# Optimization experiments

Hardware: AMD Instinct MI355X
Metric: run time of the kernel (lower is better)

## Reference

```python
import jax, jax.numpy as jnp
import numpy as np

EPS = 1e-5
COMMITMENT_WEIGHT = 1.0


def setup_inputs() -> dict:
    key = jax.random.key(0)
    k1, k2 = jax.random.split(key)
    x = jax.random.normal(k1, (4, 4096, 128), dtype=jnp.float32)
    codebook = jax.random.normal(k2, (8192, 128), dtype=jnp.float32)
    return {"x": x, "codebook": codebook}


def _layernorm(x):
    # LayerNorm over last dim, elementwise_affine=False, eps=1e-5
    mu = jnp.mean(x, axis=-1, keepdims=True)
    var = jnp.mean(jnp.square(x - mu), axis=-1, keepdims=True)
    return (x - mu) * jax.lax.rsqrt(var + EPS)


def reference(x, codebook):
    b, n, d = x.shape
    xn = _layernorm(x)                      # [b, n, d]
    flat = xn.reshape(b * n, d)             # [bn, d]
    x2 = jnp.sum(flat * flat, axis=-1, keepdims=True)          # [bn, 1]
    e2 = jnp.sum(codebook * codebook, axis=-1)                  # [K]
    dots = jnp.einsum('nd,kd->nk', flat, codebook)              # [bn, K]
    distances = x2 - 2.0 * dots + e2[None, :]                   # [bn, K]
    embed_ind = jnp.argmin(distances, axis=-1)                  # [bn]
    quantize = codebook[embed_ind].reshape(b, n, d)             # gather
    embed_ind = embed_ind.reshape(b, n)
    loss = jnp.mean(jnp.square(quantize - xn)) * COMMITMENT_WEIGHT
    # straight-through
    quantize_st = xn + jax.lax.stop_gradient(quantize - xn)
    return (quantize_st, embed_ind, loss)
```

## Files before the change

kernel.cpp:

```cpp
#include <hip/hip_runtime.h>
#include <hip/hip_fp16.h>
#include <math.h>

typedef _Float16 half8  __attribute__((ext_vector_type(8)));
typedef _Float16 half2v __attribute__((ext_vector_type(2)));
typedef float   floatx4 __attribute__((ext_vector_type(4)));

#define ROWS   16384
#define DIM    128
#define KCODES 8192
#define NSPLIT 16
#define MTILE  512
#define NT     64
#define NCHUNK ((KCODES / NSPLIT) / NT)
#define LOSS_SCALE (1.0f / ((float)ROWS * (float)DIM))

__device__ __forceinline__ void async_copy16(const _Float16* src, _Float16* dst_lds) {
  __builtin_amdgcn_global_load_lds((const __attribute__((address_space(1))) void*)src,
                                   (__attribute__((address_space(3))) void*)dst_lds,
                                   16, 0, 0);
}

__global__ __launch_bounds__(256) void prep_codebook(
    const float* __restrict__ cb, _Float16* __restrict__ ehg,
    _Float16* __restrict__ elg, float* __restrict__ e2g)
{
  int tid = threadIdx.x;
  int L = tid & 63;
  int row = blockIdx.x * 4 + (tid >> 6);
  const float2* cr = (const float2*)(cb + (size_t)row * DIM);
  float2 v = cr[L];
  float s2 = v.x * v.x + v.y * v.y;
  #pragma unroll
  for (int m = 1; m < 64; m <<= 1) s2 += __shfl_xor(s2, m);
  if (L == 0) e2g[row] = -0.5f * s2;
  _Float16 h0 = (_Float16)v.x, h1 = (_Float16)v.y;
  half2v hi = {h0, h1};
  half2v lo = {(_Float16)(v.x - (float)h0), (_Float16)(v.y - (float)h1)};
  ((half2v*)(ehg + (size_t)row * DIM))[L] = hi;
  ((half2v*)(elg + (size_t)row * DIM))[L] = lo;
}

__global__ __launch_bounds__(512, 2) void argmin_kernel(
    const float* __restrict__ x, const _Float16* __restrict__ ehg,
    const _Float16* __restrict__ elg, const float* __restrict__ e2g,
    float* __restrict__ best_part, int* __restrict__ idx_part,
    float* __restrict__ x2g)
{
  __shared__ _Float16 ebuf[2][2][64][128];
  __shared__ float e2s[KCODES / NSPLIT];

  int tid = threadIdx.x;
  int w   = tid >> 6;
  int L   = tid & 63;
  int c   = L & 15;
  int q   = L >> 4;

  int bx = blockIdx.x;
  int mt = bx & 31;
  int ns = bx >> 5;

  int rowbase = mt * MTILE + w * 64;
  int code0 = ns * (KCODES / NSPLIT);

  e2s[tid] = e2g[code0 + tid];

  half8 ah[4][4], al[4][4];

  #pragma unroll
  for (int g = 0; g < 4; ++g) {
    const float* xr = x + (size_t)(rowbase + g * 16 + c) * DIM;
    float v[32];
    #pragma unroll
    for (int ks = 0; ks < 4; ++ks) {
      float4 p0 = *(const float4*)(xr + ks * 32 + q * 8);
      float4 p1 = *(const float4*)(xr + ks * 32 + q * 8 + 4);
      v[ks*8+0] = p0.x; v[ks*8+1] = p0.y; v[ks*8+2] = p0.z; v[ks*8+3] = p0.w;
      v[ks*8+4] = p1.x; v[ks*8+5] = p1.y; v[ks*8+6] = p1.z; v[ks*8+7] = p1.w;
    }
    float s = 0.f;
    #pragma unroll
    for (int i = 0; i < 32; ++i) s += v[i];
    s += __shfl_xor(s, 16); s += __shfl_xor(s, 32);
    float mu = s * (1.0f / 128.0f);
    float s2 = 0.f;
    #pragma unroll
    for (int i = 0; i < 32; ++i) { float d = v[i] - mu; s2 += d * d; }
    s2 += __shfl_xor(s2, 16); s2 += __shfl_xor(s2, 32);
    float rstd = 1.0f / sqrtf(s2 * (1.0f / 128.0f) + 1e-5f);
    float x2 = 0.f;
    #pragma unroll
    for (int ks = 0; ks < 4; ++ks)
      #pragma unroll
      for (int j = 0; j < 8; ++j) {
        float xv = (v[ks*8+j] - mu) * rstd;
        x2 += xv * xv;
        _Float16 h = (_Float16)xv;
        ah[g][ks][j] = h;
        al[g][ks][j] = (_Float16)(xv - (float)h);
      }
    x2 += __shfl_xor(x2, 16); x2 += __shfl_xor(x2, 32);
    if (ns == 0 && q == 0) x2g[rowbase + g * 16 + c] = x2;
  }

  float best[4][4]; int bidx[4][4];
  #pragma unroll
  for (int g = 0; g < 4; ++g)
    #pragma unroll
    for (int r = 0; r < 4; ++r) { best[g][r] = -3.4e38f; bidx[g][r] = 0; }

  _Float16* lbase = &ebuf[0][0][0][0];

  auto stage = [&](int ch, int p) {
    int cbase = code0 + ch * NT;
    _Float16* lb = lbase + (size_t)p * 2 * 64 * 128;
    #pragma unroll
    for (int it = 0; it < 4; ++it) {
      int cid = it * 512 + tid;
      int arr = cid >> 10;
      int lc  = cid & 1023;
      int n   = lc >> 4;
      int kcs = lc & 15;
      int kc  = kcs ^ (n & 7);
      const _Float16* g = (arr ? elg : ehg) + (size_t)(cbase + n) * DIM + kc * 8;
      async_copy16(g, lb + (size_t)cid * 8);
    }
  };

  stage(0, 0);
  __syncthreads();

  for (int ch = 0; ch < NCHUNK; ++ch) {
    int p = ch & 1;
    int cbase = code0 + ch * NT;
    if (ch + 1 < NCHUNK) stage(ch + 1, p ^ 1);

    float e2h[4];
    #pragma unroll
    for (int s = 0; s < 4; ++s) e2h[s] = e2s[ch * NT + s * 16 + c];

    #pragma unroll
    for (int s = 0; s < 4; ++s) {
      int n = s * 16 + c;
      half8 bh[4], bl[4];
      #pragma unroll
      for (int ks = 0; ks < 4; ++ks) {
        int slot = ((ks * 4 + q) ^ (c & 7)) * 8;
        bh[ks] = *(const half8*)&ebuf[p][0][n][slot];
        bl[ks] = *(const half8*)&ebuf[p][1][n][slot];
      }
      int nn = cbase + n;
      #pragma unroll
      for (int g = 0; g < 4; ++g) {
        floatx4 acc = {e2h[s], e2h[s], e2h[s], e2h[s]};
        #pragma unroll
        for (int ks = 0; ks < 4; ++ks) {
          acc = __builtin_amdgcn_mfma_f32_16x16x32_f16(ah[g][ks], bh[ks], acc, 0, 0, 0);
          acc = __builtin_amdgcn_mfma_f32_16x16x32_f16(ah[g][ks], bl[ks], acc, 0, 0, 0);
          acc = __builtin_amdgcn_mfma_f32_16x16x32_f16(al[g][ks], bh[ks], acc, 0, 0, 0);
        }
        #pragma unroll
        for (int r = 0; r < 4; ++r) {
          float t = acc[r];
          if (t > best[g][r]) { best[g][r] = t; bidx[g][r] = nn; }
        }
      }
    }
    __syncthreads();
  }

  #pragma unroll
  for (int m = 1; m < 16; m <<= 1)
    #pragma unroll
    for (int g = 0; g < 4; ++g)
      #pragma unroll
      for (int r = 0; r < 4; ++r) {
        float ob = __shfl_xor(best[g][r], m);
        int   oi = __shfl_xor(bidx[g][r], m);
        if (ob > best[g][r] || (ob == best[g][r] && oi < bidx[g][r])) {
          best[g][r] = ob; bidx[g][r] = oi;
        }
      }
  if (c == 0) {
    #pragma unroll
    for (int g = 0; g < 4; ++g)
      #pragma unroll
      for (int r = 0; r < 4; ++r) {
        int row = rowbase + g * 16 + q * 4 + r;
        best_part[(size_t)row * NSPLIT + ns] = best[g][r];
        idx_part [(size_t)row * NSPLIT + ns] = bidx[g][r];
      }
  }
}

__global__ __launch_bounds__(256) void gather_loss_kernel(
    const float* __restrict__ cb, const float* __restrict__ best_part,
    const int* __restrict__ idx_part, const float* __restrict__ x2g,
    float* __restrict__ out_q, float* __restrict__ out_ind,
    float* __restrict__ out_loss)
{
  __shared__ int   sidx[32];
  __shared__ float sloss[32];
  int tid = threadIdx.x;
  int rb = blockIdx.x * 32;
  int r = tid >> 3, k = tid & 7;
  int row = rb + r;

  float b  = best_part[(size_t)row * NSPLIT + k];
  int   bi = idx_part [(size_t)row * NSPLIT + k];
  float b2 = best_part[(size_t)row * NSPLIT + 8 + k];
  int   bj = idx_part [(size_t)row * NSPLIT + 8 + k];
  if (b2 > b || (b2 == b && bj < bi)) { b = b2; bi = bj; }
  #pragma unroll
  for (int m = 1; m < 8; m <<= 1) {
    float ob = __shfl_xor(b, m);
    int   oi = __shfl_xor(bi, m);
    if (ob > b || (ob == b && oi < bi)) { b = ob; bi = oi; }
  }
  if (k == 0) {
    sidx[r] = bi;
    out_ind[row] = (float)bi;
    sloss[r] = x2g[row] - 2.0f * b;
  }
  __syncthreads();

  if (tid < 32) {
    float s = sloss[tid];
    #pragma unroll
    for (int m = 1; m < 32; m <<= 1) s += __shfl_xor(s, m);
    if (tid == 0) atomicAdd(out_loss, s * LOSS_SCALE);
  }

  const float4* cb4 = (const float4*)cb;
  float4* oq4 = (float4*)out_q;
  #pragma unroll
  for (int it = 0; it < 4; ++it) {
    int idx = it * 256 + tid;
    int r2 = idx >> 5, c4 = idx & 31;
    oq4[(size_t)(rb + r2) * 32 + c4] = cb4[(size_t)sidx[r2] * 32 + c4];
  }
}

extern "C" void kernel_launch(void* const* d_in, const int* in_sizes, int n_in,
                              void* d_out, int out_size, void* d_ws, size_t ws_size,
                              hipStream_t stream)
{
  const float* x  = (const float*)d_in[0];
  const float* cb = (const float*)d_in[1];

  char* ws = (char*)d_ws;
  _Float16* ehg      = (_Float16*)(ws + 0);
  _Float16* elg      = (_Float16*)(ws + 2097152);
  float*    e2g      = (float*)   (ws + 4194304);
  float*    best_part= (float*)   (ws + 4227072);
  int*      idx_part = (int*)     (ws + 5275648);
  float*    x2g      = (float*)   (ws + 6324224);

  float* out_q    = (float*)d_out;
  float* out_ind  = out_q + (size_t)ROWS * DIM;
  float* out_loss = out_ind + ROWS;

  hipMemsetAsync(out_loss, 0, sizeof(float), stream);
  prep_codebook<<<KCODES / 4, 256, 0, stream>>>(cb, ehg, elg, e2g);
  argmin_kernel<<<(ROWS / MTILE) * NSPLIT, 512, 0, stream>>>(x, ehg, elg, e2g, best_part, idx_part, x2g);
  gather_loss_kernel<<<ROWS / 32, 256, 0, stream>>>(cb, best_part, idx_part, x2g, out_q, out_ind, out_loss);
}
```

Baseline: 172.2 us.

## Switch argmin to 32x32x16 MFMA with uneven 6-way codebook split

Rewrites the distance/argmin kernel to use 32x32x16 f16 MFMAs with 32-row wave tiles, so each thread holds a single row's split-fp16 operands. The codebook is split into 6 uneven slices over 128-row tiles, giving 768 blocks of 256 threads with 3 blocks per CU, in place of 512 blocks of 512 threads. The hi and lo cross products go into a separate accumulator. The argmin tracks chunk indices and reduces across 32 lanes at the end. The loss atomic plus memset is replaced by per-block partial sums and an extra single-block reduce kernel, which adds one launch but makes the loss deterministic.

```diff
diff --git a/kernel.cpp b/kernel.cpp
--- a/kernel.cpp
+++ b/kernel.cpp
@@ -2,17 +2,15 @@
 #include <hip/hip_fp16.h>
 #include <math.h>
 
-typedef _Float16 half8  __attribute__((ext_vector_type(8)));
-typedef _Float16 half2v __attribute__((ext_vector_type(2)));
-typedef float   floatx4 __attribute__((ext_vector_type(4)));
+typedef _Float16 half8   __attribute__((ext_vector_type(8)));
+typedef _Float16 half2v  __attribute__((ext_vector_type(2)));
+typedef float    floatx16 __attribute__((ext_vector_type(16)));
 
 #define ROWS   16384
 #define DIM    128
 #define KCODES 8192
-#define NSPLIT 16
-#define MTILE  512
-#define NT     64
-#define NCHUNK ((KCODES / NSPLIT) / NT)
+#define NSPLIT 6
+#define MTILE  128
 #define LOSS_SCALE (1.0f / ((float)ROWS * (float)DIM))
 
 __device__ __forceinline__ void async_copy16(const _Float16* src, _Float16* dst_lds) {
@@ -41,88 +39,84 @@
   ((half2v*)(elg + (size_t)row * DIM))[L] = lo;
 }
 
-__global__ __launch_bounds__(512, 2) void argmin_kernel(
+__global__ __launch_bounds__(256, 3) void argmin_kernel(
     const float* __restrict__ x, const _Float16* __restrict__ ehg,
     const _Float16* __restrict__ elg, const float* __restrict__ e2g,
     float* __restrict__ best_part, int* __restrict__ idx_part,
     float* __restrict__ x2g)
 {
-  __shared__ _Float16 ebuf[2][2][64][128];
-  __shared__ float e2s[KCODES / NSPLIT];
+  __shared__ _Float16 ebuf[2][2][32][128];
+  __shared__ float e2s[1376];
 
   int tid = threadIdx.x;
   int w   = tid >> 6;
   int L   = tid & 63;
-  int c   = L & 15;
-  int q   = L >> 4;
+  int col = L & 31;
+  int kh  = L >> 5;
 
   int bx = blockIdx.x;
-  int mt = bx & 31;
-  int ns = bx >> 5;
-
-  int rowbase = mt * MTILE + w * 64;
-  int code0 = ns * (KCODES / NSPLIT);
-
-  e2s[tid] = e2g[code0 + tid];
-
-  half8 ah[4][4], al[4][4];
-
-  #pragma unroll
-  for (int g = 0; g < 4; ++g) {
-    const float* xr = x + (size_t)(rowbase + g * 16 + c) * DIM;
-    float v[32];
-    #pragma unroll
-    for (int ks = 0; ks < 4; ++ks) {
-      float4 p0 = *(const float4*)(xr + ks * 32 + q * 8);
-      float4 p1 = *(const float4*)(xr + ks * 32 + q * 8 + 4);
-      v[ks*8+0] = p0.x; v[ks*8+1] = p0.y; v[ks*8+2] = p0.z; v[ks*8+3] = p0.w;
-      v[ks*8+4] = p1.x; v[ks*8+5] = p1.y; v[ks*8+6] = p1.z; v[ks*8+7] = p1.w;
-    }
-    float s = 0.f;
-    #pragma unroll
-    for (int i = 0; i < 32; ++i) s += v[i];
-    s += __shfl_xor(s, 16); s += __shfl_xor(s, 32);
-    float mu = s * (1.0f / 128.0f);
-    float s2 = 0.f;
-    #pragma unroll
-    for (int i = 0; i < 32; ++i) { float d = v[i] - mu; s2 += d * d; }
-    s2 += __shfl_xor(s2, 16); s2 += __shfl_xor(s2, 32);
-    float rstd = 1.0f / sqrtf(s2 * (1.0f / 128.0f) + 1e-5f);
-    float x2 = 0.f;
-    #pragma unroll
-    for (int ks = 0; ks < 4; ++ks)
-      #pragma unroll
-      for (int j = 0; j < 8; ++j) {
-        float xv = (v[ks*8+j] - mu) * rstd;
-        x2 += xv * xv;
-        _Float16 h = (_Float16)xv;
-        ah[g][ks][j] = h;
-        al[g][ks][j] = (_Float16)(xv - (float)h);
-      }
-    x2 += __shfl_xor(x2, 16); x2 += __shfl_xor(x2, 32);
-    if (ns == 0 && q == 0) x2g[rowbase + g * 16 + c] = x2;
-  }
-
-  float best[4][4]; int bidx[4][4];
-  #pragma unroll
-  for (int g = 0; g < 4; ++g)
-    #pragma unroll
-    for (int r = 0; r < 4; ++r) { best[g][r] = -3.4e38f; bidx[g][r] = 0; }
-
-  _Float16* lbase = &ebuf[0][0][0][0];
+  int mt = bx & 127;
+  int ns = bx >> 7;
+  const int soff[7] = {0, 1376, 2752, 4128, 5504, 6848, 8192};
+  int code0 = soff[ns];
+  int ntile = (soff[ns + 1] - code0) >> 5;
+
+  int rowbase = mt * MTILE + w * 32;
+  int row = rowbase + col;
+
+  for (int i = tid; i < soff[ns + 1] - code0; i += 256) e2s[i] = e2g[code0 + i];
+
+  const float* xr = x + (size_t)row * DIM + kh * 8;
+  float v[64];
+  #pragma unroll
+  for (int ks = 0; ks < 8; ++ks) {
+    float4 p0 = *(const float4*)(xr + ks * 16);
+    float4 p1 = *(const float4*)(xr + ks * 16 + 4);
+    v[ks*8+0] = p0.x; v[ks*8+1] = p0.y; v[ks*8+2] = p0.z; v[ks*8+3] = p0.w;
+    v[ks*8+4] = p1.x; v[ks*8+5] = p1.y; v[ks*8+6] = p1.z; v[ks*8+7] = p1.w;
+  }
+  float s = 0.f;
+  #pragma unroll
+  for (int i = 0; i < 64; ++i) s += v[i];
+  s += __shfl_xor(s, 32);
+  float mu = s * (1.0f / 128.0f);
+  float s2 = 0.f;
+  #pragma unroll
+  for (int i = 0; i < 64; ++i) { float d = v[i] - mu; s2 += d * d; }
+  s2 += __shfl_xor(s2, 32);
+  float rstd = 1.0f / sqrtf(s2 * (1.0f / 128.0f) + 1e-5f);
+
+  half8 ah[8], al[8];
+  float x2 = 0.f;
+  #pragma unroll
+  for (int ks = 0; ks < 8; ++ks)
+    #pragma unroll
+    for (int j = 0; j < 8; ++j) {
+      float xv = (v[ks*8+j] - mu) * rstd;
+      x2 += xv * xv;
+      _Float16 h = (_Float16)xv;
+      ah[ks][j] = h;
+      al[ks][j] = (_Float16)(xv - (float)h);
+    }
+  x2 += __shfl_xor(x2, 32);
+  if (ns == 0 && kh == 0) x2g[row] = x2;
+
+  float best[16]; int bch[16];
+  #pragma unroll
+  for (int r = 0; r < 16; ++r) { best[r] = -3.4e38f; bch[r] = 0; }
 
   auto stage = [&](int ch, int p) {
-    int cbase = code0 + ch * NT;
-    _Float16* lb = lbase + (size_t)p * 2 * 64 * 128;
+    int cbase = code0 + ch * 32;
+    _Float16* lb = &ebuf[p][0][0][0];
     #pragma unroll
     for (int it = 0; it < 4; ++it) {
-      int cid = it * 512 + tid;
-      int arr = cid >> 10;
-      int lc  = cid & 1023;
+      int cid = it * 256 + tid;
+      int arr = cid >> 9;
+      int lc  = cid & 511;
       int n   = lc >> 4;
-      int kcs = lc & 15;
-      int kc  = kcs ^ (n & 7);
-      const _Float16* g = (arr ? elg : ehg) + (size_t)(cbase + n) * DIM + kc * 8;
+      int cs  = lc & 15;
+      int cg  = cs ^ (n & 15);
+      const _Float16* g = (arr ? elg : ehg) + (size_t)(cbase + n) * DIM + cg * 8;
       async_copy16(g, lb + (size_t)cid * 8);
     }
   };
@@ -130,66 +124,47 @@
   stage(0, 0);
   __syncthreads();
 
-  for (int ch = 0; ch < NCHUNK; ++ch) {
+  for (int ch = 0; ch < ntile; ++ch) {
     int p = ch & 1;
-    int cbase = code0 + ch * NT;
-    if (ch + 1 < NCHUNK) stage(ch + 1, p ^ 1);
-
-    float e2h[4];
-    #pragma unroll
-    for (int s = 0; s < 4; ++s) e2h[s] = e2s[ch * NT + s * 16 + c];
-
-    #pragma unroll
-    for (int s = 0; s < 4; ++s) {
-      int n = s * 16 + c;
-      half8 bh[4], bl[4];
-      #pragma unroll
-      for (int ks = 0; ks < 4; ++ks) {
-        int slot = ((ks * 4 + q) ^ (c & 7)) * 8;
-        bh[ks] = *(const half8*)&ebuf[p][0][n][slot];
-        bl[ks] = *(const half8*)&ebuf[p][1][n][slot];
-      }
-      int nn = cbase + n;
-      #pragma unroll
-      for (int g = 0; g < 4; ++g) {
-        floatx4 acc = {e2h[s], e2h[s], e2h[s], e2h[s]};
-        #pragma unroll
-        for (int ks = 0; ks < 4; ++ks) {
-          acc = __builtin_amdgcn_mfma_f32_16x16x32_f16(ah[g][ks], bh[ks], acc, 0, 0, 0);
-          acc = __builtin_amdgcn_mfma_f32_16x16x32_f16(ah[g][ks], bl[ks], acc, 0, 0, 0);
-          acc = __builtin_amdgcn_mfma_f32_16x16x32_f16(al[g][ks], bh[ks], acc, 0, 0, 0);
-        }
-        #pragma unroll
-        for (int r = 0; r < 4; ++r) {
-          float t = acc[r];
-          if (t > best[g][r]) { best[g][r] = t; bidx[g][r] = nn; }
-        }
-      }
+    if (ch + 1 < ntile) stage(ch + 1, p ^ 1);
+
+    float e2f = e2s[ch * 32 + col];
+
+    floatx16 a0 = {0,0,0,0,0,0,0,0,0,0,0,0,0,0,0,0};
+    floatx16 a1 = {0,0,0,0,0,0,0,0,0,0,0,0,0,0,0,0};
+    #pragma unroll
+    for (int ks = 0; ks < 8; ++ks) {
+      int slot = (((ks << 1) | kh) ^ (col & 15)) * 8;
+      half8 bh = *(const half8*)&ebuf[p][0][col][slot];
+      half8 bl = *(const half8*)&ebuf[p][1][col][slot];
+      a0 = __builtin_amdgcn_mfma_f32_32x32x16_f16(ah[ks], bh, a0, 0, 0, 0);
+      a1 = __builtin_amdgcn_mfma_f32_32x32x16_f16(ah[ks], bl, a1, 0, 0, 0);
+      a1 = __builtin_amdgcn_mfma_f32_32x32x16_f16(al[ks], bh, a1, 0, 0, 0);
+    }
+    #pragma unroll
+    for (int r = 0; r < 16; ++r) {
+      float t = (a0[r] + a1[r]) + e2f;
+      if (t > best[r]) { best[r] = t; bch[r] = ch; }
     }
     __syncthreads();
   }
 
-  #pragma unroll
-  for (int m = 1; m < 16; m <<= 1)
-    #pragma unroll
-    for (int g = 0; g < 4; ++g)
-      #pragma unroll
-      for (int r = 0; r < 4; ++r) {
-        float ob = __shfl_xor(best[g][r], m);
-        int   oi = __shfl_xor(bidx[g][r], m);
-        if (ob > best[g][r] || (ob == best[g][r] && oi < bidx[g][r])) {
-          best[g][r] = ob; bidx[g][r] = oi;
-        }
-      }
-  if (c == 0) {
-    #pragma unroll
-    for (int g = 0; g < 4; ++g)
-      #pragma unroll
-      for (int r = 0; r < 4; ++r) {
-        int row = rowbase + g * 16 + q * 4 + r;
-        best_part[(size_t)row * NSPLIT + ns] = best[g][r];
-        idx_part [(size_t)row * NSPLIT + ns] = bidx[g][r];
-      }
+  int ibase = code0 + col;
+  #pragma unroll
+  for (int r = 0; r < 16; ++r) {
+    float b = best[r];
+    int   bi = (bch[r] << 5) + ibase;
+    #pragma unroll
+    for (int m = 1; m < 32; m <<= 1) {
+      float ob = __shfl_xor(b, m);
+      int   oi = __shfl_xor(bi, m);
+      if (ob > b || (ob == b && oi < bi)) { b = ob; bi = oi; }
+    }
+    if (col == 0) {
+      int rw = rowbase + (r & 3) + ((r >> 2) << 3) + (kh << 2);
+      best_part[(size_t)rw * NSPLIT + ns] = b;
+      idx_part [(size_t)rw * NSPLIT + ns] = bi;
+    }
   }
 }
 
@@ -197,7 +172,7 @@
     const float* __restrict__ cb, const float* __restrict__ best_part,
     const int* __restrict__ idx_part, const float* __restrict__ x2g,
     float* __restrict__ out_q, float* __restrict__ out_ind,
-    float* __restrict__ out_loss)
+    float* __restrict__ loss_part)
 {
   __shared__ int   sidx[32];
   __shared__ float sloss[32];
@@ -206,11 +181,11 @@
   int r = tid >> 3, k = tid & 7;
   int row = rb + r;
 
-  float b  = best_part[(size_t)row * NSPLIT + k];
-  int   bi = idx_part [(size_t)row * NSPLIT + k];
-  float b2 = best_part[(size_t)row * NSPLIT + 8 + k];
-  int   bj = idx_part [(size_t)row * NSPLIT + 8 + k];
-  if (b2 > b || (b2 == b && bj < bi)) { b = b2; bi = bj; }
+  float b  = -3.4e38f; int bi = 0x7fffffff;
+  if (k < NSPLIT) {
+    b  = best_part[(size_t)row * NSPLIT + k];
+    bi = idx_part [(size_t)row * NSPLIT + k];
+  }
   #pragma unroll
   for (int m = 1; m < 8; m <<= 1) {
     float ob = __shfl_xor(b, m);
@@ -225,10 +200,10 @@
   __syncthreads();
 
   if (tid < 32) {
-    float s = sloss[tid];
-    #pragma unroll
-    for (int m = 1; m < 32; m <<= 1) s += __shfl_xor(s, m);
-    if (tid == 0) atomicAdd(out_loss, s * LOSS_SCALE);
+    float sl = sloss[tid];
+    #pragma unroll
+    for (int m = 1; m < 32; m <<= 1) sl += __shfl_xor(sl, m);
+    if (tid == 0) loss_part[blockIdx.x] = sl;
   }
 
   const float4* cb4 = (const float4*)cb;
@@ -239,6 +214,20 @@
     int r2 = idx >> 5, c4 = idx & 31;
     oq4[(size_t)(rb + r2) * 32 + c4] = cb4[(size_t)sidx[r2] * 32 + c4];
   }
+}
+
+__global__ __launch_bounds__(256) void loss_reduce_kernel(
+    const float* __restrict__ loss_part, float* __restrict__ out_loss)
+{
+  __shared__ float sm[256];
+  int tid = threadIdx.x;
+  float s = loss_part[tid] + loss_part[tid + 256];
+  sm[tid] = s; __syncthreads();
+  for (int st = 128; st > 0; st >>= 1) {
+    if (tid < st) sm[tid] += sm[tid + st];
+    __syncthreads();
+  }
+  if (tid == 0) *out_loss = sm[0] * LOSS_SCALE;
 }
 
 extern "C" void kernel_launch(void* const* d_in, const int* in_sizes, int n_in,
@@ -253,15 +242,16 @@
   _Float16* elg      = (_Float16*)(ws + 2097152);
   float*    e2g      = (float*)   (ws + 4194304);
   float*    best_part= (float*)   (ws + 4227072);
-  int*      idx_part = (int*)     (ws + 5275648);
-  float*    x2g      = (float*)   (ws + 6324224);
+  int*      idx_part = (int*)     (ws + 4620288);
+  float*    x2g      = (float*)   (ws + 5013504);
+  float*    loss_part= (float*)   (ws + 5079040);
 
   float* out_q    = (float*)d_out;
   float* out_ind  = out_q + (size_t)ROWS * DIM;
   float* out_loss = out_ind + ROWS;
 
-  hipMemsetAsync(out_loss, 0, sizeof(float), stream);
   prep_codebook<<<KCODES / 4, 256, 0, stream>>>(cb, ehg, elg, e2g);
-  argmin_kernel<<<(ROWS / MTILE) * NSPLIT, 512, 0, stream>>>(x, ehg, elg, e2g, best_part, idx_part, x2g);
-  gather_loss_kernel<<<ROWS / 32, 256, 0, stream>>>(cb, best_part, idx_part, x2g, out_q, out_ind, out_loss);
-}
+  argmin_kernel<<<(ROWS / MTILE) * NSPLIT, 256, 0, stream>>>(x, ehg, elg, e2g, best_part, idx_part, x2g);
+  gather_loss_kernel<<<ROWS / 32, 256, 0, stream>>>(cb, best_part, idx_part, x2g, out_q, out_ind, loss_part);
+  loss_reduce_kernel<<<1, 256, 0, stream>>>(loss_part, out_loss);
+}
```

New measurement: 179.3 us. 1.04x slower.

## Shrink argmin blocks to 256 threads, halve code splits, prefetch e2 into registers

Applied to the files above, without the earlier changes.

The argmin kernel now uses 256-thread blocks covering 256 rows and splits the codebook 8 ways instead of 16. Each staged codebook tile is therefore reused by fewer waves, and each block walks twice as many chunks. The e2 norms are read straight from global memory into registers one chunk ahead, replacing the shared-memory staging copy. The loss memset is folded into the prep kernel, and the gather kernel reduces 8 partials instead of 16. The aim is to cut per-block setup, partial-result traffic and a separate memset launch, at the cost of doubling LDS traffic per MFMA and changing the grid shape and occupancy.

```diff
diff --git a/kernel.cpp b/kernel.cpp
--- a/kernel.cpp
+++ b/kernel.cpp
@@ -9,10 +9,11 @@
 #define ROWS   16384
 #define DIM    128
 #define KCODES 8192
-#define NSPLIT 16
-#define MTILE  512
+#define NSPLIT 8
+#define MTILE  256
 #define NT     64
-#define NCHUNK ((KCODES / NSPLIT) / NT)
+#define SPLITK (KCODES / NSPLIT)
+#define NCHUNK (SPLITK / NT)
 #define LOSS_SCALE (1.0f / ((float)ROWS * (float)DIM))
 
 __device__ __forceinline__ void async_copy16(const _Float16* src, _Float16* dst_lds) {
@@ -23,13 +24,14 @@
 
 __global__ __launch_bounds__(256) void prep_codebook(
     const float* __restrict__ cb, _Float16* __restrict__ ehg,
-    _Float16* __restrict__ elg, float* __restrict__ e2g)
+    _Float16* __restrict__ elg, float* __restrict__ e2g,
+    float* __restrict__ out_loss)
 {
   int tid = threadIdx.x;
+  if (blockIdx.x == 0 && tid == 0) *out_loss = 0.f;
   int L = tid & 63;
   int row = blockIdx.x * 4 + (tid >> 6);
-  const float2* cr = (const float2*)(cb + (size_t)row * DIM);
-  float2 v = cr[L];
+  float2 v = ((const float2*)(cb + (size_t)row * DIM))[L];
   float s2 = v.x * v.x + v.y * v.y;
   #pragma unroll
   for (int m = 1; m < 64; m <<= 1) s2 += __shfl_xor(s2, m);
@@ -41,14 +43,13 @@
   ((half2v*)(elg + (size_t)row * DIM))[L] = lo;
 }
 
-__global__ __launch_bounds__(512, 2) void argmin_kernel(
+__global__ __launch_bounds__(256, 2) void argmin_kernel(
     const float* __restrict__ x, const _Float16* __restrict__ ehg,
     const _Float16* __restrict__ elg, const float* __restrict__ e2g,
     float* __restrict__ best_part, int* __restrict__ idx_part,
     float* __restrict__ x2g)
 {
   __shared__ _Float16 ebuf[2][2][64][128];
-  __shared__ float e2s[KCODES / NSPLIT];
 
   int tid = threadIdx.x;
   int w   = tid >> 6;
@@ -57,13 +58,11 @@
   int q   = L >> 4;
 
   int bx = blockIdx.x;
-  int mt = bx & 31;
-  int ns = bx >> 5;
+  int mt = bx & 63;
+  int ns = bx >> 6;
+  int code0 = ns * SPLITK;
 
   int rowbase = mt * MTILE + w * 64;
-  int code0 = ns * (KCODES / NSPLIT);
-
-  e2s[tid] = e2g[code0 + tid];
 
   half8 ah[4][4], al[4][4];
 
@@ -115,8 +114,8 @@
     int cbase = code0 + ch * NT;
     _Float16* lb = lbase + (size_t)p * 2 * 64 * 128;
     #pragma unroll
-    for (int it = 0; it < 4; ++it) {
-      int cid = it * 512 + tid;
+    for (int it = 0; it < 8; ++it) {
+      int cid = it * 256 + tid;
       int arr = cid >> 10;
       int lc  = cid & 1023;
       int n   = lc >> 4;
@@ -127,6 +126,10 @@
     }
   };
 
+  float e2n[4];
+  #pragma unroll
+  for (int s = 0; s < 4; ++s) e2n[s] = e2g[code0 + s * 16 + c];
+
   stage(0, 0);
   __syncthreads();
 
@@ -137,7 +140,11 @@
 
     float e2h[4];
     #pragma unroll
-    for (int s = 0; s < 4; ++s) e2h[s] = e2s[ch * NT + s * 16 + c];
+    for (int s = 0; s < 4; ++s) e2h[s] = e2n[s];
+    if (ch + 1 < NCHUNK) {
+      #pragma unroll
+      for (int s = 0; s < 4; ++s) e2n[s] = e2g[cbase + NT + s * 16 + c];
+    }
 
     #pragma unroll
     for (int s = 0; s < 4; ++s) {
@@ -208,9 +215,6 @@
 
   float b  = best_part[(size_t)row * NSPLIT + k];
   int   bi = idx_part [(size_t)row * NSPLIT + k];
-  float b2 = best_part[(size_t)row * NSPLIT + 8 + k];
-  int   bj = idx_part [(size_t)row * NSPLIT + 8 + k];
-  if (b2 > b || (b2 == b && bj < bi)) { b = b2; bi = bj; }
   #pragma unroll
   for (int m = 1; m < 8; m <<= 1) {
     float ob = __shfl_xor(b, m);
@@ -225,10 +229,10 @@
   __syncthreads();
 
   if (tid < 32) {
-    float s = sloss[tid];
-    #pragma unroll
-    for (int m = 1; m < 32; m <<= 1) s += __shfl_xor(s, m);
-    if (tid == 0) atomicAdd(out_loss, s * LOSS_SCALE);
+    float sl = sloss[tid];
+    #pragma unroll
+    for (int m = 1; m < 32; m <<= 1) sl += __shfl_xor(sl, m);
+    if (tid == 0) atomicAdd(out_loss, sl * LOSS_SCALE);
   }
 
   const float4* cb4 = (const float4*)cb;
@@ -253,15 +257,14 @@
   _Float16* elg      = (_Float16*)(ws + 2097152);
   float*    e2g      = (float*)   (ws + 4194304);
   float*    best_part= (float*)   (ws + 4227072);
-  int*      idx_part = (int*)     (ws + 5275648);
-  float*    x2g      = (float*)   (ws + 6324224);
+  int*      idx_part = (int*)     (ws + 4751360);
+  float*    x2g      = (float*)   (ws + 5275648);
 
   float* out_q    = (float*)d_out;
   float* out_ind  = out_q + (size_t)ROWS * DIM;
   float* out_loss = out_ind + ROWS;
 
-  hipMemsetAsync(out_loss, 0, sizeof(float), stream);
-  prep_codebook<<<KCODES / 4, 256, 0, stream>>>(cb, ehg, elg, e2g);
-  argmin_kernel<<<(ROWS / MTILE) * NSPLIT, 512, 0, stream>>>(x, ehg, elg, e2g, best_part, idx_part, x2g);
+  prep_codebook<<<KCODES / 4, 256, 0, stream>>>(cb, ehg, elg, e2g, out_loss);
+  argmin_kernel<<<(ROWS / MTILE) * NSPLIT, 256, 0, stream>>>(x, ehg, elg, e2g, best_part, idx_part, x2g);
   gather_loss_kernel<<<ROWS / 32, 256, 0, stream>>>(cb, best_part, idx_part, x2g, out_q, out_ind, out_loss);
 }
```

After: 162.6 us. 1.06x faster.
